# Optimization experiments

Measured on AMD Instinct MI355X. Metric: run time of the kernel, lower is better.

## Reference

```python
import jax, jax.numpy as jnp
import numpy as np

EPS = 1e-12  # matches torch F.normalize default eps


def _l2norm(x):
    n = jnp.linalg.norm(x, axis=-1, keepdims=True)
    return x / jnp.maximum(n, EPS)


def setup_inputs() -> dict:
    key = jax.random.key(0)
    k1, k2 = jax.random.split(key)
    B, Na, T, Nv, D = 16, 128, 10, 196, 256
    audio_feats = jax.random.normal(k1, (B, Na, D), dtype=jnp.float32)
    visual_feats = jax.random.normal(k2, (B, T, Nv, D), dtype=jnp.float32)
    temperature = jnp.asarray(2.0, dtype=jnp.float32)
    return {"audio_feats": audio_feats, "visual_feats": visual_feats,
            "temperature": temperature}


def reference(audio_feats, visual_feats, temperature):
    # audio_feats: (B, Na, D); visual_feats: (B, T, Nv, D)
    a = _l2norm(audio_feats)                         # (B, Na, D)
    v = _l2norm(visual_feats)                        # (B, T, Nv, D)
    # all-pairs token-level cosine sims: (Bx, By, Na, T, Nv)
    sims = jnp.einsum('xad,ytvd->xyatv', a, v) / temperature
    # aggregate: max over patches, mean over time, mean over audio tokens
    clip_sims = sims.max(axis=-1).mean(axis=-1).mean(axis=-1)  # (B, B)

    # InfoNCE on diagonal
    B = clip_sims.shape[0]
    diag = jnp.arange(B)
    log_p_a2v = jax.nn.log_softmax(clip_sims, axis=1)
    log_p_v2a = jax.nn.log_softmax(clip_sims.T, axis=1)
    losses = -(log_p_a2v[diag, diag] + log_p_v2a[diag, diag])
    contrastive_loss = 0.5 * losses.mean()

    # regularization: non-negativity pressure + temperature band [1, 3]
    neg = jnp.minimum(sims, 0.0)
    l_nonneg = jnp.mean(neg * neg)
    log_t = jnp.log(temperature)
    temp_low = jnp.maximum(-log_t, 0.0) ** 4
    temp_high = jnp.maximum(log_t - jnp.log(3.0), 0.0) ** 4
    reg_loss = l_nonneg + temp_low + temp_high

    total_loss = contrastive_loss + 0.3 * reg_loss
    return (total_loss, contrastive_loss, reg_loss)
```

## Files before the change

### kernel.cpp

```cpp
#include <hip/hip_runtime.h>
#include <stdint.h>


typedef __bf16 bf16x8 __attribute__((ext_vector_type(8)));
typedef float  f32x16 __attribute__((ext_vector_type(16)));

#define WS_A_OFF  ((size_t)0)
#define WS_V_OFF  ((size_t)(1u<<20))
#define WS_CP_OFF (WS_V_OFF + (size_t)16*2560*512)

#define NINF (-3.4e38f)

__device__ __forceinline__ int fenc(float f) {
    int i = __float_as_int(f);
    return i >= 0 ? i : (i ^ 0x7fffffff);
}
__device__ __forceinline__ float fdec(int i) {
    return __int_as_float(i >= 0 ? i : (i ^ 0x7fffffff));
}
__device__ __forceinline__ void gld_lds16(const char* g, char* l) {
    __builtin_amdgcn_global_load_lds(
        (const __attribute__((address_space(1))) void*)g,
        (__attribute__((address_space(3))) void*)l, 16, 0, 0);
}

__global__ __launch_bounds__(256) void prep_kernel(const float* __restrict__ audio,
                                                   const float* __restrict__ visual,
                                                   char* __restrict__ ws)
{
    const int wave = blockIdx.x * 4 + (threadIdx.x >> 6);
    const int lane = threadIdx.x & 63;
    const int g    = lane >> 4;
    const int sub  = lane & 15;
    const int row  = wave * 4 + g;

    float4 v0 = {0,0,0,0}, v1 = {0,0,0,0}, v2 = {0,0,0,0}, v3 = {0,0,0,0};
    size_t dst0, dst1;
    if (row < 2048) {
        const float* s = audio + (size_t)row * 256 + sub * 16;
        v0 = *(const float4*)(s);  v1 = *(const float4*)(s + 4);
        v2 = *(const float4*)(s + 8); v3 = *(const float4*)(s + 12);
        dst0 = WS_A_OFF + (size_t)row * 512 + sub * 32;
        dst1 = dst0 + 16;
    } else {
        const int vr  = row - 2048;
        const int y   = vr / 2560;
        const int rem = vr - y * 2560;
        const int t   = rem >> 8;
        const int vv  = rem & 255;
        if (vv < 196) {
            const float* s = visual + (size_t)((y*10 + t)*196 + vv) * 256 + sub * 16;
            v0 = *(const float4*)(s);  v1 = *(const float4*)(s + 4);
            v2 = *(const float4*)(s + 8); v3 = *(const float4*)(s + 12);
        }
        const size_t base = WS_V_OFF + (size_t)vr * 512;
        const int u0 = (2*sub)     ^ (vr & 7);
        const int u1 = (2*sub + 1) ^ (vr & 7);
        dst0 = base + ((size_t)u0 << 4);
        dst1 = base + ((size_t)u1 << 4);
    }

    float ss = v0.x*v0.x + v0.y*v0.y + v0.z*v0.z + v0.w*v0.w
             + v1.x*v1.x + v1.y*v1.y + v1.z*v1.z + v1.w*v1.w
             + v2.x*v2.x + v2.y*v2.y + v2.z*v2.z + v2.w*v2.w
             + v3.x*v3.x + v3.y*v3.y + v3.z*v3.z + v3.w*v3.w;
    #pragma unroll
    for (int m = 1; m < 16; m <<= 1) ss += __shfl_xor(ss, m);
    const float sc = 1.0f / fmaxf(sqrtf(ss), 1e-12f);

    bf16x8 oa, ob;
    oa[0]=(__bf16)(v0.x*sc); oa[1]=(__bf16)(v0.y*sc); oa[2]=(__bf16)(v0.z*sc); oa[3]=(__bf16)(v0.w*sc);
    oa[4]=(__bf16)(v1.x*sc); oa[5]=(__bf16)(v1.y*sc); oa[6]=(__bf16)(v1.z*sc); oa[7]=(__bf16)(v1.w*sc);
    ob[0]=(__bf16)(v2.x*sc); ob[1]=(__bf16)(v2.y*sc); ob[2]=(__bf16)(v2.z*sc); ob[3]=(__bf16)(v2.w*sc);
    ob[4]=(__bf16)(v3.x*sc); ob[5]=(__bf16)(v3.y*sc); ob[6]=(__bf16)(v3.z*sc); ob[7]=(__bf16)(v3.w*sc);
    *(uint4*)(ws + dst0) = __builtin_bit_cast(uint4, oa);
    *(uint4*)(ws + dst1) = __builtin_bit_cast(uint4, ob);
}

#define STAGE(c_, buf_) do {                                          \
    const char* s_ = vbase + (size_t)(c_) * 32768 + tid * 16;         \
    char* d_ = smem + ((buf_) << 15) + tid * 16;                      \
    gld_lds16(s_,         d_);         gld_lds16(s_ +  4096, d_ +  4096); \
    gld_lds16(s_ +  8192, d_ +  8192); gld_lds16(s_ + 12288, d_ + 12288); \
    gld_lds16(s_ + 16384, d_ + 16384); gld_lds16(s_ + 20480, d_ + 20480); \
    gld_lds16(s_ + 24576, d_ + 24576); gld_lds16(s_ + 28672, d_ + 28672); \
} while (0)

__global__ __launch_bounds__(256, 2) void main_kernel(char* __restrict__ ws)
{
    extern __shared__ __align__(16) char smem[];
    __shared__ int part_lds[640];
    __shared__ float red[8];

    const int tid  = threadIdx.x;
    const int lane = tid & 63;
    const int wid  = tid >> 6;
    const int aw   = wid & 1;
    const int vw   = wid >> 1;
    const int l31  = lane & 31;
    const int hi   = lane >> 5;

    const int b = blockIdx.x;
    const int xcd = b & 7, slot = b >> 3;
    const int y = xcd * 2 + (slot >> 5);
    const int x = (slot >> 1) & 15;
    const int h = slot & 1;

    for (int i = tid; i < 640; i += 256) part_lds[i] = (int)0x80000000;

    bf16x8 af0[16], af1[16];
    {
        const char* ab = ws + WS_A_OFF + (size_t)(x*128 + aw*64) * 512;
        #pragma unroll
        for (int k = 0; k < 16; ++k) {
            af0[k] = __builtin_bit_cast(bf16x8,
                *(const uint4*)(ab + l31*512 + k*32 + hi*16));
            af1[k] = __builtin_bit_cast(bf16x8,
                *(const uint4*)(ab + (32 + l31)*512 + k*32 + hi*16));
        }
    }
    asm volatile("s_waitcnt vmcnt(0)" ::: "memory");

    const char* vbase = ws + WS_V_OFF + ((size_t)y * 2560 + (size_t)h * 1280) * 512;

    float nn = 0.f, rmax0 = NINF, rmax1 = NINF;

    STAGE(0, 0);

    for (int c = 0; c < 20; ++c) {
        if (c < 19) {
            STAGE(c + 1, (c + 1) & 1);
            asm volatile("s_waitcnt vmcnt(8)" ::: "memory");
        } else {
            asm volatile("s_waitcnt vmcnt(0)" ::: "memory");
        }
        __builtin_amdgcn_s_barrier();

        const int f  = 2*c + vw;
        const int ft = f & 7;
        if (ft != 7) {
            const char* bb = smem + ((c & 1) << 15) + ((vw*32 + l31) * 512);
            const int sx = (l31 & 7) << 4;

            f32x16 acc0 = {}, acc1 = {};
            #pragma unroll
            for (int hf = 0; hf < 2; ++hf) {
                bf16x8 vf[8];
                #pragma unroll
                for (int k8 = 0; k8 < 8; ++k8) {
                    const int u = (((hf*8 + k8)*2 + hi) << 4) ^ sx;
                    vf[k8] = __builtin_bit_cast(bf16x8, *(const uint4*)(bb + u));
                }
                #pragma unroll
                for (int k8 = 0; k8 < 8; ++k8) {
                    acc0 = __builtin_amdgcn_mfma_f32_32x32x16_bf16(vf[k8], af0[hf*8 + k8], acc0, 0,0,0);
                    acc1 = __builtin_amdgcn_mfma_f32_32x32x16_bf16(vf[k8], af1[hf*8 + k8], acc1, 0,0,0);
                }
            }

            #pragma unroll
            for (int i = 0; i < 16; ++i) {
                const float g0 = fminf(acc0[i], 0.f);
                const float g1 = fminf(acc1[i], 0.f);
                nn = fmaf(g0, g0, nn);
                nn = fmaf(g1, g1, nn);
            }
            float m0, m1;
            if (ft == 6) {
                m0 = fmaxf(fmaxf(acc0[0], acc0[1]), fmaxf(acc0[2], acc0[3]));
                m1 = fmaxf(fmaxf(acc1[0], acc1[1]), fmaxf(acc1[2], acc1[3]));
                if (hi) { m0 = NINF; m1 = NINF; }
            } else {
                float a0 = fmaxf(fmaxf(acc0[0], acc0[1]), fmaxf(acc0[2], acc0[3]));
                float a1 = fmaxf(fmaxf(acc0[4], acc0[5]), fmaxf(acc0[6], acc0[7]));
                float a2 = fmaxf(fmaxf(acc0[8], acc0[9]), fmaxf(acc0[10], acc0[11]));
                float a3 = fmaxf(fmaxf(acc0[12], acc0[13]), fmaxf(acc0[14], acc0[15]));
                m0 = fmaxf(fmaxf(a0, a1), fmaxf(a2, a3));
                float b0 = fmaxf(fmaxf(acc1[0], acc1[1]), fmaxf(acc1[2], acc1[3]));
                float b1 = fmaxf(fmaxf(acc1[4], acc1[5]), fmaxf(acc1[6], acc1[7]));
                float b2 = fmaxf(fmaxf(acc1[8], acc1[9]), fmaxf(acc1[10], acc1[11]));
                float b3 = fmaxf(fmaxf(acc1[12], acc1[13]), fmaxf(acc1[14], acc1[15]));
                m1 = fmaxf(fmaxf(b0, b1), fmaxf(b2, b3));
            }
            rmax0 = fmaxf(rmax0, m0);
            rmax1 = fmaxf(rmax1, m1);
        }

        if ((c & 3) == 3) {
            const int tl = c >> 2;
            float vv0 = fmaxf(rmax0, __shfl_xor(rmax0, 32));
            float vv1 = fmaxf(rmax1, __shfl_xor(rmax1, 32));
            if (hi == 0) {
                atomicMax(&part_lds[(aw*64 + l31) * 5 + tl],      fenc(vv0));
                atomicMax(&part_lds[(aw*64 + 32 + l31) * 5 + tl], fenc(vv1));
            }
            rmax0 = NINF; rmax1 = NINF;
        }
        asm volatile("" ::: "memory");
        __builtin_amdgcn_s_barrier();
    }

    __syncthreads();

    float sum = 0.f;
    for (int i = tid; i < 640; i += 256) sum += fdec(part_lds[i]);
    #pragma unroll
    for (int m = 1; m < 64; m <<= 1) {
        sum += __shfl_xor(sum, m);
        nn  += __shfl_xor(nn, m);
    }
    if (lane == 0) { red[wid] = sum; red[4 + wid] = nn; }
    __syncthreads();
    if (tid == 0) {
        float S = 0.f, N = 0.f;
        #pragma unroll
        for (int w = 0; w < 4; ++w) { S += red[w]; N += red[4 + w]; }
        float* cp = (float*)(ws + WS_CP_OFF);
        cp[(x*16 + y)*2 + h]       = S;
        cp[512 + (x*16 + y)*2 + h] = N;
    }
}

__global__ void final_kernel(const char* __restrict__ ws,
                             const float* __restrict__ temp,
                             float* __restrict__ out)
{
    __shared__ float cs[16][17];
    __shared__ float nnred[256];
    __shared__ float lse_r[16], lse_c[16];
    const int tid = threadIdx.x;
    const float T = temp[0];
    const float* cp = (const float*)(ws + WS_CP_OFF);
    cs[tid >> 4][tid & 15] = (cp[tid*2] + cp[tid*2 + 1]) / (1280.0f * T);
    nnred[tid] = cp[512 + tid*2] + cp[512 + tid*2 + 1];
    __syncthreads();
    for (int s = 128; s > 0; s >>= 1) {
        if (tid < s) nnred[tid] += nnred[tid + s];
        __syncthreads();
    }
    if (tid < 16) {
        float m = NINF;
        for (int j = 0; j < 16; ++j) m = fmaxf(m, cs[tid][j]);
        float s = 0.f;
        for (int j = 0; j < 16; ++j) s += expf(cs[tid][j] - m);
        lse_r[tid] = m + logf(s);
    } else if (tid < 32) {
        const int c = tid - 16;
        float m = NINF;
        for (int j = 0; j < 16; ++j) m = fmaxf(m, cs[j][c]);
        float s = 0.f;
        for (int j = 0; j < 16; ++j) s += expf(cs[j][c] - m);
        lse_c[c] = m + logf(s);
    }
    __syncthreads();
    if (tid == 0) {
        float acc = 0.f;
        for (int i = 0; i < 16; ++i)
            acc += (lse_r[i] - cs[i][i]) + (lse_c[i] - cs[i][i]);
        const float contrastive = 0.5f * acc * (1.0f / 16.0f);
        const float l_nonneg = nnred[0] / (64225280.0f * T * T);
        const float lt = logf(T);
        float tl = fmaxf(-lt, 0.f); tl = tl * tl; tl = tl * tl;
        float th = fmaxf(lt - 1.0986122886681098f, 0.f); th = th * th; th = th * th;
        const float reg = l_nonneg + tl + th;
        out[0] = contrastive + 0.3f * reg;
        out[1] = contrastive;
        out[2] = reg;
    }
}

extern "C" void kernel_launch(void* const* d_in, const int* in_sizes, int n_in,
                              void* d_out, int out_size, void* d_ws, size_t ws_size,
                              hipStream_t stream)
{
    const float* audio  = (const float*)d_in[0];
    const float* visual = (const float*)d_in[1];
    const float* temp   = (const float*)d_in[2];
    char* ws = (char*)d_ws;

    prep_kernel<<<2688, 256, 0, stream>>>(audio, visual, ws);
    main_kernel<<<512, 256, 65536, stream>>>(ws);
    final_kernel<<<1, 256, 0, stream>>>(ws, temp, (float*)d_out);
}
```

Measured before the change: 128.4 us.

## Switch normalized features to FP8 and use fp8 MFMA with smaller tiles

Normalized audio and visual rows are now stored as FP8 (e4m3) instead of bf16, which halves workspace traffic and LDS staging. The main kernel uses the 32x32x16 fp8 MFMA with one accumulator per wave and half the audio rows per block, and launches twice as many blocks at higher occupancy (4 blocks/CU, static 32KB LDS). The LDS swizzle is adapted to 8-byte granules and the final kernel now sums four partials per clip pair. FP8 rounding lowers the precision of the cosine similarities, so it risks tolerance errors in the max/mean aggregation and in the non-negativity term.

```diff
diff --git a/kernel.cpp b/kernel.cpp
--- a/kernel.cpp
+++ b/kernel.cpp
@@ -2,12 +2,11 @@
 #include <stdint.h>
 
 
-typedef __bf16 bf16x8 __attribute__((ext_vector_type(8)));
-typedef float  f32x16 __attribute__((ext_vector_type(16)));
+typedef float f32x16 __attribute__((ext_vector_type(16)));
 
 #define WS_A_OFF  ((size_t)0)
 #define WS_V_OFF  ((size_t)(1u<<20))
-#define WS_CP_OFF (WS_V_OFF + (size_t)16*2560*512)
+#define WS_CP_OFF (WS_V_OFF + (size_t)16*2560*256)
 
 #define NINF (-3.4e38f)
 
@@ -30,18 +29,19 @@
 {
     const int wave = blockIdx.x * 4 + (threadIdx.x >> 6);
     const int lane = threadIdx.x & 63;
-    const int g    = lane >> 4;
-    const int sub  = lane & 15;
-    const int row  = wave * 4 + g;
-
-    float4 v0 = {0,0,0,0}, v1 = {0,0,0,0}, v2 = {0,0,0,0}, v3 = {0,0,0,0};
-    size_t dst0, dst1;
+    const int half = lane >> 5;
+    const int sub  = lane & 31;
+    const int row  = wave * 2 + half;
+
+    float f[8];
+    #pragma unroll
+    for (int i = 0; i < 8; ++i) f[i] = 0.f;
+    size_t dst;
     if (row < 2048) {
-        const float* s = audio + (size_t)row * 256 + sub * 16;
-        v0 = *(const float4*)(s);  v1 = *(const float4*)(s + 4);
-        v2 = *(const float4*)(s + 8); v3 = *(const float4*)(s + 12);
-        dst0 = WS_A_OFF + (size_t)row * 512 + sub * 32;
-        dst1 = dst0 + 16;
+        const float* s = audio + (size_t)row * 256 + sub * 8;
+        *(float4*)(f)     = *(const float4*)(s);
+        *(float4*)(f + 4) = *(const float4*)(s + 4);
+        dst = WS_A_OFF + (size_t)row * 256 + sub * 8;
     } else {
         const int vr  = row - 2048;
         const int y   = vr / 2560;
@@ -49,47 +49,38 @@
         const int t   = rem >> 8;
         const int vv  = rem & 255;
         if (vv < 196) {
-            const float* s = visual + (size_t)((y*10 + t)*196 + vv) * 256 + sub * 16;
-            v0 = *(const float4*)(s);  v1 = *(const float4*)(s + 4);
-            v2 = *(const float4*)(s + 8); v3 = *(const float4*)(s + 12);
-        }
-        const size_t base = WS_V_OFF + (size_t)vr * 512;
-        const int u0 = (2*sub)     ^ (vr & 7);
-        const int u1 = (2*sub + 1) ^ (vr & 7);
-        dst0 = base + ((size_t)u0 << 4);
-        dst1 = base + ((size_t)u1 << 4);
-    }
-
-    float ss = v0.x*v0.x + v0.y*v0.y + v0.z*v0.z + v0.w*v0.w
-             + v1.x*v1.x + v1.y*v1.y + v1.z*v1.z + v1.w*v1.w
-             + v2.x*v2.x + v2.y*v2.y + v2.z*v2.z + v2.w*v2.w
-             + v3.x*v3.x + v3.y*v3.y + v3.z*v3.z + v3.w*v3.w;
-    #pragma unroll
-    for (int m = 1; m < 16; m <<= 1) ss += __shfl_xor(ss, m);
+            const float* s = visual + (size_t)((y*10 + t)*196 + vv) * 256 + sub * 8;
+            *(float4*)(f)     = *(const float4*)(s);
+            *(float4*)(f + 4) = *(const float4*)(s + 4);
+        }
+        dst = WS_V_OFF + (size_t)vr * 256 + (size_t)((sub ^ (vr & 31)) << 3);
+    }
+
+    float ss = 0.f;
+    #pragma unroll
+    for (int i = 0; i < 8; ++i) ss += f[i] * f[i];
+    #pragma unroll
+    for (int m = 1; m < 32; m <<= 1) ss += __shfl_xor(ss, m);
     const float sc = 1.0f / fmaxf(sqrtf(ss), 1e-12f);
 
-    bf16x8 oa, ob;
-    oa[0]=(__bf16)(v0.x*sc); oa[1]=(__bf16)(v0.y*sc); oa[2]=(__bf16)(v0.z*sc); oa[3]=(__bf16)(v0.w*sc);
-    oa[4]=(__bf16)(v1.x*sc); oa[5]=(__bf16)(v1.y*sc); oa[6]=(__bf16)(v1.z*sc); oa[7]=(__bf16)(v1.w*sc);
-    ob[0]=(__bf16)(v2.x*sc); ob[1]=(__bf16)(v2.y*sc); ob[2]=(__bf16)(v2.z*sc); ob[3]=(__bf16)(v2.w*sc);
-    ob[4]=(__bf16)(v3.x*sc); ob[5]=(__bf16)(v3.y*sc); ob[6]=(__bf16)(v3.z*sc); ob[7]=(__bf16)(v3.w*sc);
-    *(uint4*)(ws + dst0) = __builtin_bit_cast(uint4, oa);
-    *(uint4*)(ws + dst1) = __builtin_bit_cast(uint4, ob);
+    int w0 = __builtin_amdgcn_cvt_pk_fp8_f32(f[0]*sc, f[1]*sc, 0, false);
+    w0     = __builtin_amdgcn_cvt_pk_fp8_f32(f[2]*sc, f[3]*sc, w0, true);
+    int w1 = __builtin_amdgcn_cvt_pk_fp8_f32(f[4]*sc, f[5]*sc, 0, false);
+    w1     = __builtin_amdgcn_cvt_pk_fp8_f32(f[6]*sc, f[7]*sc, w1, true);
+    *(uint2*)(ws + dst) = make_uint2((unsigned)w0, (unsigned)w1);
 }
 
 #define STAGE(c_, buf_) do {                                          \
-    const char* s_ = vbase + (size_t)(c_) * 32768 + tid * 16;         \
-    char* d_ = smem + ((buf_) << 15) + tid * 16;                      \
+    const char* s_ = vbase + (size_t)(c_) * 16384 + tid * 16;         \
+    char* d_ = &smem[buf_][0] + tid * 16;                             \
     gld_lds16(s_,         d_);         gld_lds16(s_ +  4096, d_ +  4096); \
     gld_lds16(s_ +  8192, d_ +  8192); gld_lds16(s_ + 12288, d_ + 12288); \
-    gld_lds16(s_ + 16384, d_ + 16384); gld_lds16(s_ + 20480, d_ + 20480); \
-    gld_lds16(s_ + 24576, d_ + 24576); gld_lds16(s_ + 28672, d_ + 28672); \
 } while (0)
 
-__global__ __launch_bounds__(256, 2) void main_kernel(char* __restrict__ ws)
-{
-    extern __shared__ __align__(16) char smem[];
-    __shared__ int part_lds[640];
+__global__ __launch_bounds__(256, 4) void main_kernel(char* __restrict__ ws)
+{
+    __shared__ __align__(16) char smem[2][16384];
+    __shared__ int part[320];
     __shared__ float red[8];
 
     const int tid  = threadIdx.x;
@@ -101,36 +92,33 @@
     const int hi   = lane >> 5;
 
     const int b = blockIdx.x;
-    const int xcd = b & 7, slot = b >> 3;
-    const int y = xcd * 2 + (slot >> 5);
-    const int x = (slot >> 1) & 15;
-    const int h = slot & 1;
-
-    for (int i = tid; i < 640; i += 256) part_lds[i] = (int)0x80000000;
-
-    bf16x8 af0[16], af1[16];
+    const int xcd = b & 7, s = b >> 3;
+    const int y  = xcd * 2 + (s >> 6);
+    const int x2 = (s & 63) >> 1;
+    const int h  = s & 1;
+
+    for (int i = tid; i < 320; i += 256) part[i] = (int)0x80000000;
+
+    uint64_t af[16];
     {
-        const char* ab = ws + WS_A_OFF + (size_t)(x*128 + aw*64) * 512;
+        const char* ab = ws + WS_A_OFF + (size_t)(x2*64 + aw*32 + l31) * 256 + hi*8;
         #pragma unroll
-        for (int k = 0; k < 16; ++k) {
-            af0[k] = __builtin_bit_cast(bf16x8,
-                *(const uint4*)(ab + l31*512 + k*32 + hi*16));
-            af1[k] = __builtin_bit_cast(bf16x8,
-                *(const uint4*)(ab + (32 + l31)*512 + k*32 + hi*16));
-        }
+        for (int k = 0; k < 16; ++k)
+            af[k] = *(const uint64_t*)(ab + k*16);
     }
     asm volatile("s_waitcnt vmcnt(0)" ::: "memory");
-
-    const char* vbase = ws + WS_V_OFF + ((size_t)y * 2560 + (size_t)h * 1280) * 512;
-
-    float nn = 0.f, rmax0 = NINF, rmax1 = NINF;
+    __syncthreads();
+
+    const char* vbase = ws + WS_V_OFF + ((size_t)y * 2560 + (size_t)h * 1280) * 256;
+
+    float nn = 0.f, rmax = NINF;
 
     STAGE(0, 0);
 
     for (int c = 0; c < 20; ++c) {
         if (c < 19) {
             STAGE(c + 1, (c + 1) & 1);
-            asm volatile("s_waitcnt vmcnt(8)" ::: "memory");
+            asm volatile("s_waitcnt vmcnt(4)" ::: "memory");
         } else {
             asm volatile("s_waitcnt vmcnt(0)" ::: "memory");
         }
@@ -139,62 +127,43 @@
         const int f  = 2*c + vw;
         const int ft = f & 7;
         if (ft != 7) {
-            const char* bb = smem + ((c & 1) << 15) + ((vw*32 + l31) * 512);
-            const int sx = (l31 & 7) << 4;
-
-            f32x16 acc0 = {}, acc1 = {};
+            const char* bb = &smem[c & 1][0] + (vw*32 + l31) * 256;
+            uint64_t vf[16];
             #pragma unroll
-            for (int hf = 0; hf < 2; ++hf) {
-                bf16x8 vf[8];
-                #pragma unroll
-                for (int k8 = 0; k8 < 8; ++k8) {
-                    const int u = (((hf*8 + k8)*2 + hi) << 4) ^ sx;
-                    vf[k8] = __builtin_bit_cast(bf16x8, *(const uint4*)(bb + u));
-                }
-                #pragma unroll
-                for (int k8 = 0; k8 < 8; ++k8) {
-                    acc0 = __builtin_amdgcn_mfma_f32_32x32x16_bf16(vf[k8], af0[hf*8 + k8], acc0, 0,0,0);
-                    acc1 = __builtin_amdgcn_mfma_f32_32x32x16_bf16(vf[k8], af1[hf*8 + k8], acc1, 0,0,0);
-                }
-            }
+            for (int k = 0; k < 16; ++k)
+                vf[k] = *(const uint64_t*)(bb + (((k*2 + hi) ^ l31) << 3));
+
+            f32x16 acc = {};
+            #pragma unroll
+            for (int k = 0; k < 16; ++k)
+                acc = __builtin_amdgcn_mfma_f32_32x32x16_fp8_fp8(
+                    (long)vf[k], (long)af[k], acc, 0, 0, 0);
 
             #pragma unroll
             for (int i = 0; i < 16; ++i) {
-                const float g0 = fminf(acc0[i], 0.f);
-                const float g1 = fminf(acc1[i], 0.f);
-                nn = fmaf(g0, g0, nn);
-                nn = fmaf(g1, g1, nn);
+                const float g = fminf(acc[i], 0.f);
+                nn = fmaf(g, g, nn);
             }
-            float m0, m1;
+            float m;
             if (ft == 6) {
-                m0 = fmaxf(fmaxf(acc0[0], acc0[1]), fmaxf(acc0[2], acc0[3]));
-                m1 = fmaxf(fmaxf(acc1[0], acc1[1]), fmaxf(acc1[2], acc1[3]));
-                if (hi) { m0 = NINF; m1 = NINF; }
+                m = fmaxf(fmaxf(acc[0], acc[1]), fmaxf(acc[2], acc[3]));
+                if (hi) m = NINF;
             } else {
-                float a0 = fmaxf(fmaxf(acc0[0], acc0[1]), fmaxf(acc0[2], acc0[3]));
-                float a1 = fmaxf(fmaxf(acc0[4], acc0[5]), fmaxf(acc0[6], acc0[7]));
-                float a2 = fmaxf(fmaxf(acc0[8], acc0[9]), fmaxf(acc0[10], acc0[11]));
-                float a3 = fmaxf(fmaxf(acc0[12], acc0[13]), fmaxf(acc0[14], acc0[15]));
-                m0 = fmaxf(fmaxf(a0, a1), fmaxf(a2, a3));
-                float b0 = fmaxf(fmaxf(acc1[0], acc1[1]), fmaxf(acc1[2], acc1[3]));
-                float b1 = fmaxf(fmaxf(acc1[4], acc1[5]), fmaxf(acc1[6], acc1[7]));
-                float b2 = fmaxf(fmaxf(acc1[8], acc1[9]), fmaxf(acc1[10], acc1[11]));
-                float b3 = fmaxf(fmaxf(acc1[12], acc1[13]), fmaxf(acc1[14], acc1[15]));
-                m1 = fmaxf(fmaxf(b0, b1), fmaxf(b2, b3));
+                float a0 = fmaxf(fmaxf(acc[0], acc[1]),   fmaxf(acc[2], acc[3]));
+                float a1 = fmaxf(fmaxf(acc[4], acc[5]),   fmaxf(acc[6], acc[7]));
+                float a2 = fmaxf(fmaxf(acc[8], acc[9]),   fmaxf(acc[10], acc[11]));
+                float a3 = fmaxf(fmaxf(acc[12], acc[13]), fmaxf(acc[14], acc[15]));
+                m = fmaxf(fmaxf(a0, a1), fmaxf(a2, a3));
             }
-            rmax0 = fmaxf(rmax0, m0);
-            rmax1 = fmaxf(rmax1, m1);
+            rmax = fmaxf(rmax, m);
         }
 
         if ((c & 3) == 3) {
             const int tl = c >> 2;
-            float vv0 = fmaxf(rmax0, __shfl_xor(rmax0, 32));
-            float vv1 = fmaxf(rmax1, __shfl_xor(rmax1, 32));
-            if (hi == 0) {
-                atomicMax(&part_lds[(aw*64 + l31) * 5 + tl],      fenc(vv0));
-                atomicMax(&part_lds[(aw*64 + 32 + l31) * 5 + tl], fenc(vv1));
-            }
-            rmax0 = NINF; rmax1 = NINF;
+            float v = fmaxf(rmax, __shfl_xor(rmax, 32));
+            if (hi == 0)
+                atomicMax(&part[(aw*32 + l31) * 5 + tl], fenc(v));
+            rmax = NINF;
         }
         asm volatile("" ::: "memory");
         __builtin_amdgcn_s_barrier();
@@ -203,7 +172,7 @@
     __syncthreads();
 
     float sum = 0.f;
-    for (int i = tid; i < 640; i += 256) sum += fdec(part_lds[i]);
+    for (int i = tid; i < 320; i += 256) sum += fdec(part[i]);
     #pragma unroll
     for (int m = 1; m < 64; m <<= 1) {
         sum += __shfl_xor(sum, m);
@@ -216,8 +185,9 @@
         #pragma unroll
         for (int w = 0; w < 4; ++w) { S += red[w]; N += red[4 + w]; }
         float* cp = (float*)(ws + WS_CP_OFF);
-        cp[(x*16 + y)*2 + h]       = S;
-        cp[512 + (x*16 + y)*2 + h] = N;
+        const int idx = (x2*16 + y)*2 + h;
+        cp[idx]        = S;
+        cp[1024 + idx] = N;
     }
 }
 
@@ -231,8 +201,18 @@
     const int tid = threadIdx.x;
     const float T = temp[0];
     const float* cp = (const float*)(ws + WS_CP_OFF);
-    cs[tid >> 4][tid & 15] = (cp[tid*2] + cp[tid*2 + 1]) / (1280.0f * T);
-    nnred[tid] = cp[512 + tid*2] + cp[512 + tid*2 + 1];
+    const int x = tid >> 4, yy = tid & 15;
+    float sclip = 0.f;
+    #pragma unroll
+    for (int a = 0; a < 2; ++a)
+        #pragma unroll
+        for (int hh = 0; hh < 2; ++hh)
+            sclip += cp[(((2*x + a)*16 + yy)*2) + hh];
+    cs[x][yy] = sclip / (1280.0f * T);
+    float n = 0.f;
+    #pragma unroll
+    for (int j = 0; j < 4; ++j) n += cp[1024 + tid + j*256];
+    nnred[tid] = n;
     __syncthreads();
     for (int s = 128; s > 0; s >>= 1) {
         if (tid < s) nnred[tid] += nnred[tid + s];
@@ -278,7 +258,7 @@
     const float* temp   = (const float*)d_in[2];
     char* ws = (char*)d_ws;
 
-    prep_kernel<<<2688, 256, 0, stream>>>(audio, visual, ws);
-    main_kernel<<<512, 256, 65536, stream>>>(ws);
+    prep_kernel<<<5376, 256, 0, stream>>>(audio, visual, ws);
+    main_kernel<<<1024, 256, 0, stream>>>(ws);
     final_kernel<<<1, 256, 0, stream>>>(ws, temp, (float*)d_out);
 }
```

After: 121.5 us. -5.4%, faster.
